# Optimization experiments

Hardware: AMD Instinct MI355X
Metric: run time of the kernel (lower is better)

## Reference

```python
import jax, jax.numpy as jnp
import numpy as np

D = 512          # descriptor_dim
H = 8            # num_heads
HD = D // H      # per-head dim
L = 12           # GNN layers: ['self','cross']*6
NAMES = ['self', 'cross'] * 6
SINKHORN_ITERS = 100
IN_EPS = 1e-5    # InstanceNorm1d eps


def _conv1x1(W, b, x):
    # W: [o, d], b: [o], x: [b, d, n] -> [b, o, n]  (1x1 Conv1d)
    return jnp.einsum('od,bdn->bon', W, x) + b[:, None]


def _instance_norm(x):
    # InstanceNorm1d(affine=False): normalize each (batch, channel) over n
    mean = jnp.mean(x, axis=-1, keepdims=True)
    var = jnp.mean(jnp.square(x - mean), axis=-1, keepdims=True)  # biased
    return (x - mean) * jax.lax.rsqrt(var + IN_EPS)


def _mha(x, src, Wq, bq, Wk, bk, Wv, bv, Wm, bm):
    # x, src: [b, D, n] / [b, D, m]; fused head-major QKV projections
    b, _, n = x.shape
    m = src.shape[2]
    q = _conv1x1(Wq, bq, x).reshape(b, H, HD, n)
    k = _conv1x1(Wk, bk, src).reshape(b, H, HD, m)
    v = _conv1x1(Wv, bv, src).reshape(b, H, HD, m)
    scores = jnp.einsum('bhdn,bhdm->bhnm', q, k) / np.float32(np.sqrt(HD))
    prob = jax.nn.softmax(scores, axis=-1)
    out = jnp.einsum('bhnm,bhdm->bhdn', prob, v)      # [b, h, hd, n]
    # torch stacks heads at dim=2 -> [b, hd, h, n], then views (b, hd*h, n):
    out = out.transpose(0, 2, 1, 3).reshape(b, D, n)  # dim-major merge order
    return _conv1x1(Wm, bm, out)


def _prop_layer(x, src, Wq, bq, Wk, bk, Wv, bv, Wm, bm, W1, b1, W2, b2):
    # AttentionalPropagation: attn message + MLP([2D, 2D, D]) with InstanceNorm
    msg = _mha(x, src, Wq, bq, Wk, bk, Wv, bv, Wm, bm)
    y = jnp.concatenate([x, msg], axis=1)             # [b, 2D, n]
    z = jax.nn.relu(_instance_norm(_conv1x1(W1, b1, y)))
    return _conv1x1(W2, b2, z)                        # [b, D, n]


def _log_optimal_transport(scores, alpha, iters):
    b, m, n = scores.shape
    ms = jnp.asarray(m, scores.dtype)
    ns = jnp.asarray(n, scores.dtype)
    bins0 = jnp.broadcast_to(alpha, (b, m, 1))
    bins1 = jnp.broadcast_to(alpha, (b, 1, n))
    a = jnp.broadcast_to(alpha, (b, 1, 1))
    couplings = jnp.concatenate(
        [jnp.concatenate([scores, bins0], -1),
         jnp.concatenate([bins1, a], -1)], 1)         # [b, m+1, n+1]
    norm = -jnp.log(ms + ns)
    log_mu = jnp.concatenate([jnp.full((m,), norm), (jnp.log(ns) + norm)[None]])
    log_nu = jnp.concatenate([jnp.full((n,), norm), (jnp.log(ms) + norm)[None]])
    log_mu = jnp.broadcast_to(log_mu, (b, m + 1))
    log_nu = jnp.broadcast_to(log_nu, (b, n + 1))

    def step(carry, _):
        u, v = carry
        u = log_mu - jax.scipy.special.logsumexp(couplings + v[:, None, :], axis=2)
        v = log_nu - jax.scipy.special.logsumexp(couplings + u[:, :, None], axis=1)
        return (u, v), None

    (u, v), _ = jax.lax.scan(
        step, (jnp.zeros_like(log_mu), jnp.zeros_like(log_nu)), None,
        length=iters)
    return couplings + u[:, :, None] + v[:, None, :] - norm


def setup_inputs() -> dict:
    key = jax.random.key(0)
    ks = jax.random.split(key, 12)
    B, N0, N1 = 4, 1024, 1024
    s = np.float32(0.03)  # ~1/sqrt(D) init scale for stability over 12 layers

    def p(k, shape):
        return jax.random.normal(k, shape, jnp.float32) * s

    return {
        'descs_0': jax.random.normal(ks[0], (B, N0, D), jnp.float32),
        'descs_1': jax.random.normal(ks[1], (B, N1, D), jnp.float32),
        'Wq': p(ks[2], (L, D, D)), 'bq': jnp.zeros((L, D), jnp.float32),
        'Wk': p(ks[3], (L, D, D)), 'bk': jnp.zeros((L, D), jnp.float32),
        'Wv': p(ks[4], (L, D, D)), 'bv': jnp.zeros((L, D), jnp.float32),
        'Wm': p(ks[5], (L, D, D)), 'bm': jnp.zeros((L, D), jnp.float32),
        'W1': p(ks[6], (L, 2 * D, 2 * D)), 'b1': jnp.zeros((L, 2 * D), jnp.float32),
        'W2': p(ks[7], (L, D, 2 * D)), 'b2': jnp.zeros((L, D), jnp.float32),
        'Wf': p(ks[8], (D, D)), 'bf': jnp.zeros((D,), jnp.float32),
        'bin_score': jnp.asarray(1.0, jnp.float32),
    }


def reference(descs_0, descs_1, Wq, bq, Wk, bk, Wv, bv, Wm, bm,
              W1, b1, W2, b2, Wf, bf, bin_score):
    # [B, N, D] -> channels-first [B, D, N]
    x0 = jnp.transpose(descs_0, (0, 2, 1))
    x1 = jnp.transpose(descs_1, (0, 2, 1))
    for i, name in enumerate(NAMES):
        s0, s1 = (x1, x0) if name == 'cross' else (x0, x1)
        args = (Wq[i], bq[i], Wk[i], bk[i], Wv[i], bv[i], Wm[i], bm[i],
                W1[i], b1[i], W2[i], b2[i])
        d0 = _prop_layer(x0, s0, *args)
        d1 = _prop_layer(x1, s1, *args)
        x0 = x0 + d0
        x1 = x1 + d1
    m0 = _conv1x1(Wf, bf, x0)
    m1 = _conv1x1(Wf, bf, x1)
    scores = jnp.einsum('bdn,bdm->bnm', m0, m1) / np.float32(np.sqrt(D))
    return _log_optimal_transport(scores, bin_score, SINKHORN_ITERS)
```

## Files before the change

kernel.cpp:

```cpp
#include <hip/hip_runtime.h>
#include <hip/hip_bf16.h>
#include <hip/hip_fp16.h>
#include <cmath>

using bf16 = __hip_bfloat16;
typedef __attribute__((ext_vector_type(8))) short short8;
typedef __attribute__((ext_vector_type(4))) short shortx4;
typedef __attribute__((ext_vector_type(4))) float floatx4;
typedef unsigned long long u64t;

__device__ __forceinline__ void lds_load16(void* lds, const void* g) {
  __builtin_amdgcn_global_load_lds(
      (const __attribute__((address_space(1))) void*)g,
      (__attribute__((address_space(3))) void*)lds, 16, 0, 0);
}

struct GemmP {
  const bf16* A; const bf16* B;
  int M, N, K, lda, ldb;
  long sAimg, sAh, sBimg, sBh;
  int ZH, cross;
  float scale;
  const float* bias;
  float* Cf; int ldcf; long sCfImg, sCfH;
  bf16* Cb; int ldcb; long sCbImg, sCbH;
  __half* Ch; int ldch; long sChImg, sChH;
  const float* resid;
  bf16* Cv; int vColOfs;
  float* statsOut;
};

template <int NTILE>
__global__ __launch_bounds__(256, 2)
void gemm_bt(GemmP p) {
  __shared__ __align__(16) bf16 As[128 * 32];
  __shared__ __align__(16) bf16 Bs[NTILE * 32];
  constexpr int MI = (NTILE == 128) ? 4 : 2;
  const int z = blockIdx.z;
  const int imgA = z / p.ZH;
  const int h = z - imgA * p.ZH;
  const int imgB = imgA ^ p.cross;
  const bf16* Ab = p.A + (long)imgA * p.sAimg + (long)h * p.sAh;
  const bf16* Bb = p.B + (long)imgB * p.sBimg + (long)h * p.sBh;
  const int m0 = blockIdx.y * 128, n0 = blockIdx.x * NTILE;
  const int t = threadIdx.x, w = t >> 6, l = t & 63;
  const int lr = l >> 2, lk = (l & 3) * 8;
  const int fr = l & 15, fk = (l >> 4) * 8;

  const bf16* aG0 = Ab + (long)(m0 + w * 16 + lr) * p.lda + lk;
  const bf16* aG1 = aG0 + (long)64 * p.lda;
  const bf16* bG0 = Bb + (long)(n0 + w * 16 + lr) * p.ldb + lk;
  const bf16* bG1 = bG0 + (long)64 * p.ldb;
  bf16* aL0 = &As[w * 16 * 32];
  bf16* aL1 = &As[(w + 4) * 16 * 32];
  bf16* bL0 = &Bs[w * 16 * 32];
  bf16* bL1 = &Bs[(w + 4) * 16 * 32];
  const int wr = (NTILE == 128) ? (w >> 1) * 64 : w * 32;
  const int wc = (NTILE == 128) ? (w & 1) * 64 : 0;

  floatx4 zero4 = {0.f, 0.f, 0.f, 0.f};
  floatx4 acc[MI][4];
#pragma unroll
  for (int i = 0; i < MI; i++)
#pragma unroll
    for (int j = 0; j < 4; j++) acc[i][j] = zero4;

  for (int k0 = 0; k0 < p.K; k0 += 32) {
    lds_load16(aL0, aG0 + k0);
    lds_load16(aL1, aG1 + k0);
    lds_load16(bL0, bG0 + k0);
    if (NTILE == 128) lds_load16(bL1, bG1 + k0);
    __syncthreads();
    short8 af[MI], bfv[4];
#pragma unroll
    for (int i = 0; i < MI; i++)
      af[i] = *(const short8*)&As[(wr + i * 16 + fr) * 32 + fk];
#pragma unroll
    for (int j = 0; j < 4; j++)
      bfv[j] = *(const short8*)&Bs[(wc + j * 16 + fr) * 32 + fk];
#pragma unroll
    for (int i = 0; i < MI; i++)
#pragma unroll
      for (int j = 0; j < 4; j++)
        acc[i][j] = __builtin_amdgcn_mfma_f32_16x16x32_bf16(af[i], bfv[j], acc[i][j], 0, 0, 0);
    __syncthreads();
  }

  const int cl = l & 15, rq = (l >> 4) * 4;
  const long cfBase = (long)imgA * p.sCfImg + (long)h * p.sCfH;
  const long cbBase = (long)imgA * p.sCbImg + (long)h * p.sCbH;
  const long chBase = (long)imgA * p.sChImg + (long)h * p.sChH;
#pragma unroll
  for (int j = 0; j < 4; j++) {
    const int col = n0 + wc + j * 16 + cl;
    if (col >= p.N) continue;
    const float bv = p.bias ? p.bias[col] : 0.f;
    const bool vcol = p.Cv && (col >= p.vColOfs);
    float cs = 0.f, cs2 = 0.f;
#pragma unroll
    for (int i = 0; i < MI; i++) {
      float vr[4];
#pragma unroll
      for (int r = 0; r < 4; r++) {
        const int row = m0 + wr + i * 16 + rq + r;
        float val = acc[i][j][r] * p.scale + bv;
        if (p.resid) val += p.resid[cfBase + (long)row * p.ldcf + col];
        if (p.Cf) p.Cf[cfBase + (long)row * p.ldcf + col] = val;
        if (p.Cb && !vcol) p.Cb[cbBase + (long)row * p.ldcb + col] = __float2bfloat16(val);
        if (p.Ch) p.Ch[chBase + (long)row * p.ldch + col] = __float2half(val);
        if (p.statsOut) { cs += val; cs2 += val * val; }
        vr[r] = val;
      }
      if (vcol) {
        const int row0 = m0 + wr + i * 16 + rq;
        const int img = row0 >> 10, tok = row0 & 1023;
        const int ch = col - p.vColOfs;
        shortx4 pk;
#pragma unroll
        for (int r = 0; r < 4; r++) {
          bf16 bb = __float2bfloat16(vr[r]);
          pk[r] = *reinterpret_cast<short*>(&bb);
        }
        *(shortx4*)(p.Cv + (long)img * 524288 + (long)ch * 1024 + tok) = pk;
      }
    }
    if (p.statsOut) {
      cs += __shfl_xor(cs, 16); cs += __shfl_xor(cs, 32);
      cs2 += __shfl_xor(cs2, 16); cs2 += __shfl_xor(cs2, 32);
      if (l < 16) {
        const int img = m0 >> 10;
        atomicAdd(&p.statsOut[img * 2048 + col], cs);
        atomicAdd(&p.statsOut[img * 2048 + 1024 + col], cs2);
      }
    }
  }
}

__global__ __launch_bounds__(256, 4)
void attn_fused(const bf16* __restrict__ QKV, const bf16* __restrict__ vchan,
                bf16* __restrict__ Yb, int cross) {
  __shared__ __align__(16) bf16 Qs[64 * 64];
  __shared__ __align__(16) bf16 Ks[64 * 64];
  __shared__ __align__(16) bf16 Vs[64 * 64];
  __shared__ __align__(16) bf16 Ps[64 * 64];
  const int z = blockIdx.z;
  const int img = z >> 3, h = z & 7;
  const int imgB = img ^ cross;
  const int q0 = blockIdx.x * 64;
  const int t = threadIdx.x, w = t >> 6, l = t & 63;
  const int g = l >> 4, fr = l & 15;
  const int wr = w * 16;

  {
    const bf16* src = QKV + ((long)(img * 1024 + q0)) * 1536 + h * 64;
#pragma unroll
    for (int k = 0; k < 2; k++) {
      const int chunk = t + k * 256;
      const int row = chunk >> 3, c16 = chunk & 7;
      const short8 vd = *(const short8*)(src + (long)row * 1536 + c16 * 8);
      *(short8*)((char*)Qs + row * 128 + ((c16 * 16) ^ ((row & 7) << 4))) = vd;
    }
  }
  __syncthreads();

  short8 qf[2];
#pragma unroll
  for (int ks = 0; ks < 2; ks++) {
    const int row = wr + fr;
    qf[ks] = *(const short8*)((const char*)Qs + row * 128 +
                              ((ks * 64 + g * 16) ^ ((row & 7) << 4)));
  }

  floatx4 zero4 = {0.f, 0.f, 0.f, 0.f};
  floatx4 Oa[4];
  float m_run[4], l_run[4];
#pragma unroll
  for (int r = 0; r < 4; r++) { m_run[r] = -3.0e38f; l_run[r] = 0.f; }
#pragma unroll
  for (int jd = 0; jd < 4; jd++) Oa[jd] = zero4;

  const bf16* ksrc0 = QKV + ((long)(imgB * 1024)) * 1536 + 512 + h * 64;
  const bf16* vsrc0 = vchan + (long)imgB * 524288 + (long)(h * 64) * 1024;

  for (int kv = 0; kv < 16; kv++) {
    const int kv0 = kv * 64;
#pragma unroll
    for (int k = 0; k < 2; k++) {
      const int ch = t + k * 256;
      const int row = ch >> 3, c16 = ch & 7;
      const short8 vd = *(const short8*)(ksrc0 + (long)(kv0 + row) * 1536 + c16 * 8);
      *(short8*)((char*)Ks + row * 128 + ((c16 * 16) ^ ((row & 7) << 4))) = vd;
    }
#pragma unroll
    for (int k = 0; k < 2; k++) {
      const int ch = t + k * 256;
      const int row = ch >> 3, c16 = ch & 7;
      const short8 vd = *(const short8*)(vsrc0 + (long)row * 1024 + kv0 + c16 * 8);
      *(short8*)((char*)Vs + row * 128 + ((c16 * 16) ^ ((row & 7) << 4))) = vd;
    }
    __syncthreads();

    floatx4 sa[4];
#pragma unroll
    for (int j = 0; j < 4; j++) {
      sa[j] = zero4;
      const int row = j * 16 + fr;
      const short8 bk0 = *(const short8*)((const char*)Ks + row * 128 +
                                          ((g * 16) ^ ((row & 7) << 4)));
      const short8 bk1 = *(const short8*)((const char*)Ks + row * 128 +
                                          ((64 + g * 16) ^ ((row & 7) << 4)));
      sa[j] = __builtin_amdgcn_mfma_f32_16x16x32_bf16(qf[0], bk0, sa[j], 0, 0, 0);
      sa[j] = __builtin_amdgcn_mfma_f32_16x16x32_bf16(qf[1], bk1, sa[j], 0, 0, 0);
    }

#pragma unroll
    for (int r = 0; r < 4; r++) {
      float mx = -3.0e38f;
#pragma unroll
      for (int j = 0; j < 4; j++) {
        sa[j][r] *= 0.125f;
        mx = fmaxf(mx, sa[j][r]);
      }
#pragma unroll
      for (int o = 1; o < 16; o <<= 1) mx = fmaxf(mx, __shfl_xor(mx, o));
      const float mnew = fmaxf(m_run[r], mx);
      const float corr = __expf(m_run[r] - mnew);
      m_run[r] = mnew;
      float ps = 0.f;
#pragma unroll
      for (int j = 0; j < 4; j++) {
        const float pv = __expf(sa[j][r] - mnew);
        sa[j][r] = pv;
        ps += pv;
      }
#pragma unroll
      for (int o = 1; o < 16; o <<= 1) ps += __shfl_xor(ps, o);
      l_run[r] = l_run[r] * corr + ps;
#pragma unroll
      for (int jd = 0; jd < 4; jd++) Oa[jd][r] *= corr;
    }

#pragma unroll
    for (int j = 0; j < 4; j++)
#pragma unroll
      for (int r = 0; r < 4; r++) {
        const int row = wr + g * 4 + r;
        const int colB = j * 32 + fr * 2;
        *(bf16*)((char*)Ps + row * 128 + (colB ^ ((row & 7) << 4))) =
            __float2bfloat16(sa[j][r]);
      }

    short8 pf[2];
#pragma unroll
    for (int ks = 0; ks < 2; ks++) {
      const int row = wr + fr;
      pf[ks] = *(const short8*)((const char*)Ps + row * 128 +
                                ((ks * 64 + g * 16) ^ ((row & 7) << 4)));
    }
#pragma unroll
    for (int jd = 0; jd < 4; jd++) {
      const int row = jd * 16 + fr;
      const short8 vf0 = *(const short8*)((const char*)Vs + row * 128 +
                                          ((g * 16) ^ ((row & 7) << 4)));
      const short8 vf1 = *(const short8*)((const char*)Vs + row * 128 +
                                          ((64 + g * 16) ^ ((row & 7) << 4)));
      Oa[jd] = __builtin_amdgcn_mfma_f32_16x16x32_bf16(pf[0], vf0, Oa[jd], 0, 0, 0);
      Oa[jd] = __builtin_amdgcn_mfma_f32_16x16x32_bf16(pf[1], vf1, Oa[jd], 0, 0, 0);
    }
    __syncthreads();
  }

#pragma unroll
  for (int r = 0; r < 4; r++) {
    const float inv = 1.f / l_run[r];
    const int qrow = q0 + wr + g * 4 + r;
    bf16* dst = Yb + ((long)img * 1024 + qrow) * 1024 + 512 + h * 64;
#pragma unroll
    for (int jd = 0; jd < 4; jd++)
      dst[jd * 16 + fr] = __float2bfloat16(Oa[jd][r] * inv);
  }
}

__global__ __launch_bounds__(256)
void cvt_f2b(const float* __restrict__ in, bf16* __restrict__ out, long n) {
  long i = (long)blockIdx.x * 256 + threadIdx.x;
  const long stride = (long)gridDim.x * 256;
  for (; i < n; i += stride) out[i] = __float2bfloat16(in[i]);
}

__global__ __launch_bounds__(256)
void cvt_prep(const float* __restrict__ W1, const float* __restrict__ Wm,
              bf16* __restrict__ w1r, bf16* __restrict__ wmT) {
  const long i = (long)blockIdx.x * 256 + threadIdx.x;
  if (i < 6291456L) {
    const int lay = (int)(i >> 19);
    const long r = i & 524287;
    const int o = (int)(r >> 9), k = (int)(r & 511);
    w1r[i] = __float2bfloat16(W1[(long)lay * 1048576 + (long)o * 1024 + 512 + k]);
  } else if (i < 9437184L) {
    const long j = i - 6291456L;
    const int lay = (int)(j >> 18);
    const long r = j & 262143;
    const int c = (int)(r >> 9), ii = (int)(r & 511);
    wmT[j] = __float2bfloat16(Wm[(long)lay * 262144 + (long)ii * 512 + (c & 63) * 8 + (c >> 6)]);
  }
}

__global__ __launch_bounds__(256)
void bc_calc(const float* __restrict__ W1, const float* __restrict__ bm,
             const float* __restrict__ b1, float* __restrict__ bc) {
  const int w = threadIdx.x >> 6, l = threadIdx.x & 63;
  const int og = blockIdx.x * 4 + w;
  const int lay = og >> 10, o = og & 1023;
  const float* wrow = W1 + (long)lay * 1048576 + (long)o * 1024 + 512;
  const float* bmr = bm + lay * 512;
  float s = 0.f;
#pragma unroll
  for (int j = 0; j < 8; j++) s += wrow[l + 64 * j] * bmr[l + 64 * j];
#pragma unroll
  for (int o2 = 32; o2 >= 1; o2 >>= 1) s += __shfl_xor(s, o2);
  if (l == 0) bc[og] = b1[og] + s;
}

__global__ __launch_bounds__(256)
void cvt_layer(const float* __restrict__ Wq, const float* __restrict__ Wk,
               const float* __restrict__ Wv, const float* __restrict__ W1,
               const float* __restrict__ W2, const bf16* __restrict__ wcAll,
               const float* __restrict__ bq, const float* __restrict__ bk,
               const float* __restrict__ bv,
               int layer, bf16* __restrict__ out, float* __restrict__ bqkv) {
  const long i = (long)blockIdx.x * 256 + threadIdx.x;
  if (i >= 2359296L + 1536) return;
  if (i >= 2359296L) {
    const int j = (int)(i - 2359296L);
    float b;
    if (j < 512) b = bq[layer * 512 + j];
    else if (j < 1024) b = bk[layer * 512 + j - 512];
    else b = bv[layer * 512 + j - 1024];
    bqkv[j] = b;
    return;
  }
  if (i < 786432) {
    float v;
    if (i < 262144) v = Wq[(long)layer * 262144 + i];
    else if (i < 524288) v = Wk[(long)layer * 262144 + i - 262144];
    else v = Wv[(long)layer * 262144 + i - 524288];
    out[i] = __float2bfloat16(v);
  } else if (i < 1835008) {
    const long j = i - 786432;
    const int o = (int)(j >> 10), k = (int)(j & 1023);
    if (k < 512)
      out[i] = __float2bfloat16(W1[(long)layer * 1048576 + (long)o * 1024 + k]);
    else
      out[i] = wcAll[(long)layer * 524288 + (long)o * 512 + (k - 512)];
  } else {
    const long j = i - 1835008;
    out[i] = __float2bfloat16(W2[(long)layer * 524288 + j]);
  }
}

__global__ __launch_bounds__(256)
void init_x(const float* __restrict__ d0, const float* __restrict__ d1,
            float* __restrict__ Xf, bf16* __restrict__ Yb) {
  long i = (long)blockIdx.x * 256 + threadIdx.x;
  const long stride = (long)gridDim.x * 256;
  const long n = 8L * 1024 * 512;
  for (; i < n; i += stride) {
    const int d = (int)(i & 511);
    const long nn = i >> 9;
    const int img = (int)(nn >> 10);
    const int row = (int)(nn & 1023);
    const int b = img >> 1, s = img & 1;
    const float v = (s ? d1 : d0)[((long)b * 1024 + row) * 512 + d];
    Xf[i] = v;
    Yb[(nn << 10) + d] = __float2bfloat16(v);
  }
}

__global__ __launch_bounds__(256)
void in_apply(const float* __restrict__ T1, const float* __restrict__ stats,
              bf16* __restrict__ Z) {
  long i = (long)blockIdx.x * 256 + threadIdx.x;
  const long stride = (long)gridDim.x * 256;
  for (; i < 8L * 1024 * 1024; i += stride) {
    const int c = (int)(i & 1023);
    const int img = (int)(i >> 20);
    const float mean = stats[img * 2048 + c] * (1.f / 1024.f);
    const float var = fmaxf(stats[img * 2048 + 1024 + c] * (1.f / 1024.f) - mean * mean, 0.f);
    const float zz = (T1[i] - mean) * rsqrtf(var + 1e-5f);
    Z[i] = __float2bfloat16(fmaxf(zz, 0.f));
  }
}

__global__ __launch_bounds__(256)
void coup_to_fp16(float* __restrict__ io, const float* __restrict__ alpha,
                  __half* __restrict__ outN, __half* __restrict__ outT) {
  __shared__ float tile[32][33];
  const float a = *alpha;
  const int b = blockIdx.z;
  const int x0 = blockIdx.x * 32, y0 = blockIdx.y * 32;
  const int lx = threadIdx.x & 31, ly = threadIdx.x >> 5;
#pragma unroll
  for (int i = 0; i < 4; i++) {
    const int y = ly + i * 8;
    if (y0 + y < 1025 && x0 + lx < 1025) {
      const long idx = ((long)b * 1025 + y0 + y) * 1025 + x0 + lx;
      const bool edge = (y0 + y == 1024) || (x0 + lx == 1024);
      float vv;
      if (edge) { vv = a; io[idx] = a; }
      else vv = io[idx];
      tile[y][lx] = vv;
      outN[idx] = __float2half(vv);
    }
  }
  __syncthreads();
#pragma unroll
  for (int i = 0; i < 4; i++) {
    const int y = ly + i * 8;
    if (x0 + y < 1025 && y0 + lx < 1025)
      outT[((long)b * 1025 + x0 + y) * 1025 + y0 + lx] = __float2half(tile[lx][y]);
  }
}

#define SK_BLOCKS 256

#define SK_ROUND(CREG, CLAST, XREG, XLAST, SRC, DST)                            \
  {                                                                             \
    u64t pr;                                                                    \
    while ((unsigned)((pr = __hip_atomic_load(&(SRC)[t], __ATOMIC_RELAXED,      \
                                              __HIP_MEMORY_SCOPE_AGENT)) >>    \
                      32) != tag)                                               \
      __builtin_amdgcn_s_sleep(1);                                              \
    sv[t] = __uint_as_float((unsigned)pr);                                      \
    if (t == 0) {                                                               \
      u64t qr;                                                                  \
      while ((unsigned)((qr = __hip_atomic_load(&(SRC)[1024], __ATOMIC_RELAXED, \
                                                __HIP_MEMORY_SCOPE_AGENT)) >>  \
                        32) != tag)                                             \
        __builtin_amdgcn_s_sleep(1);                                            \
      sv[1024] = __uint_as_float((unsigned)qr);                                 \
    }                                                                           \
    __syncthreads();                                                            \
    float M = (l == 0) ? ((CLAST) + sv[1024]) : -3.0e38f;                       \
    const float extra = M;                                                      \
    float x[16];                                                                \
    _Pragma("unroll") for (int i = 0; i < 16; i++) {                            \
      x[i] = (CREG)[i] + sv[l + 64 * i];                                        \
      M = fmaxf(M, x[i]);                                                       \
    }                                                                           \
    _Pragma("unroll") for (int o = 32; o >= 1; o >>= 1)                         \
        M = fmaxf(M, __shfl_xor(M, o));                                         \
    float S = (l == 0) ? __expf(extra - M) : 0.f;                               \
    _Pragma("unroll") for (int i = 0; i < 16; i++) S += __expf(x[i] - M);       \
    _Pragma("unroll") for (int o = 32; o >= 1; o >>= 1) S += __shfl_xor(S, o);  \
    if (l == 0) {                                                               \
      const float val = norm - (M + __logf(S));                                 \
      const u64t pk = ((u64t)(tag + 1) << 32) | (u64t)__float_as_uint(val);     \
      __hip_atomic_store(&(DST)[lw], pk, __ATOMIC_RELAXED,                      \
                         __HIP_MEMORY_SCOPE_AGENT);                             \
    }                                                                           \
    if (xtra) {                                                                 \
      float M2 = (l == 0) ? ((XLAST) + sv[1024]) : -3.0e38f;                    \
      const float e2 = M2;                                                      \
      float y[16];                                                              \
      _Pragma("unroll") for (int i = 0; i < 16; i++) {                          \
        y[i] = (XREG)[i] + sv[l + 64 * i];                                      \
        M2 = fmaxf(M2, y[i]);                                                   \
      }                                                                         \
      _Pragma("unroll") for (int o = 32; o >= 1; o >>= 1)                       \
          M2 = fmaxf(M2, __shfl_xor(M2, o));                                    \
      float S2 = (l == 0) ? __expf(e2 - M2) : 0.f;                              \
      _Pragma("unroll") for (int i = 0; i < 16; i++) S2 += __expf(y[i] - M2);   \
      _Pragma("unroll") for (int o = 32; o >= 1; o >>= 1)                       \
          S2 += __shfl_xor(S2, o);                                              \
      if (l == 0) {                                                             \
        const float v2 = (logN + norm) - (M2 + __logf(S2));                     \
        const u64t pk2 = ((u64t)(tag + 1) << 32) | (u64t)__float_as_uint(v2);   \
        __hip_atomic_store(&(DST)[1024], pk2, __ATOMIC_RELAXED,                 \
                           __HIP_MEMORY_SCOPE_AGENT);                           \
      }                                                                         \
    }                                                                           \
    tag++;                                                                      \
    __syncthreads();                                                            \
  }

__global__ __launch_bounds__(1024)
void sinkhorn_pers(const __half* __restrict__ C, const __half* __restrict__ CT,
                   u64t* __restrict__ u, u64t* __restrict__ v,
                   float norm, float logN, int iters) {
  __shared__ float sv[1025];
  const int t = threadIdx.x;
  const int w = t >> 6, l = t & 63;
  const int b = blockIdx.x >> 6;
  const int kb = blockIdx.x & 63;
  const int lw = kb * 16 + w;
  const __half* Cb = C + (long)b * 1050625;
  const __half* CTb = CT + (long)b * 1050625;
  u64t* ub = u + b * 1025;
  u64t* vb = v + b * 1025;

  float cr[16], cc[16];
  float clC, clT;
  {
    const __half* rc = Cb + (long)lw * 1025;
    const __half* rt = CTb + (long)lw * 1025;
#pragma unroll
    for (int i = 0; i < 16; i++) {
      cr[i] = __half2float(rc[l + 64 * i]);
      cc[i] = __half2float(rt[l + 64 * i]);
    }
    clC = (l == 0) ? __half2float(rc[1024]) : 0.f;
    clT = (l == 0) ? __half2float(rt[1024]) : 0.f;
  }
  const bool xtra = (lw == 0);
  float xrC[16], xrT[16], xlC = 0.f, xlT = 0.f;
  if (xtra) {
    const __half* rc = Cb + (long)1024 * 1025;
    const __half* rt = CTb + (long)1024 * 1025;
#pragma unroll
    for (int i = 0; i < 16; i++) {
      xrC[i] = __half2float(rc[l + 64 * i]);
      xrT[i] = __half2float(rt[l + 64 * i]);
    }
    if (l == 0) {
      xlC = __half2float(rc[1024]);
      xlT = __half2float(rt[1024]);
    }
  }

  unsigned tag = 0;
  for (int it = 0; it < iters; it++) {
    SK_ROUND(cr, clC, xrC, xlC, vb, ub);
    SK_ROUND(cc, clT, xrT, xlT, ub, vb);
  }
}

__global__ __launch_bounds__(256)
void ot_final(float* __restrict__ C, const u64t* __restrict__ u,
              const u64t* __restrict__ v, float norm) {
  long i = (long)blockIdx.x * 256 + threadIdx.x;
  if (i >= 4L * 1025 * 1025) return;
  const int b = (int)(i / 1050625);
  const long r = i - (long)b * 1050625;
  const int n = (int)(r / 1025);
  const int m = (int)(r - (long)n * 1025);
  const float uu = __uint_as_float((unsigned)u[b * 1025 + n]);
  const float vv = __uint_as_float((unsigned)v[b * 1025 + m]);
  C[i] += uu + vv - norm;
}

extern "C" void kernel_launch(void* const* d_in, const int* in_sizes, int n_in,
                              void* d_out, int out_size, void* d_ws, size_t ws_size,
                              hipStream_t stream) {
  (void)in_sizes; (void)n_in; (void)out_size; (void)ws_size;
  const float* descs0 = (const float*)d_in[0];
  const float* descs1 = (const float*)d_in[1];
  const float* Wq = (const float*)d_in[2];
  const float* bq = (const float*)d_in[3];
  const float* Wk = (const float*)d_in[4];
  const float* bk = (const float*)d_in[5];
  const float* Wv = (const float*)d_in[6];
  const float* bvv = (const float*)d_in[7];
  const float* Wm = (const float*)d_in[8];
  const float* bm = (const float*)d_in[9];
  const float* W1 = (const float*)d_in[10];
  const float* b1 = (const float*)d_in[11];
  const float* W2 = (const float*)d_in[12];
  const float* b2 = (const float*)d_in[13];
  const float* Wf = (const float*)d_in[14];
  const float* bff = (const float*)d_in[15];
  const float* alpha = (const float*)d_in[16];

  char* ws = (char*)d_ws;
  size_t off = 0;
  auto alloc = [&](size_t bytes) -> void* {
    off = (off + 255) & ~(size_t)255;
    void* p = ws + off;
    off += bytes;
    return p;
  };

  bf16* wL = (bf16*)alloc(2359296L * 2);
  float* bqkv = (float*)alloc(1536 * 4);
  bf16* WfB = (bf16*)alloc(512L * 512 * 2);
  bf16* wcAll = (bf16*)alloc(12L * 1024 * 512 * 2);
  float* bcAll = (float*)alloc(12L * 1024 * 4);
  float* Xf = (float*)alloc(8L * 1024 * 512 * 4);
  bf16* Yb = (bf16*)alloc(8L * 1024 * 1024 * 2);
  bf16* QKVb = (bf16*)alloc(8L * 1024 * 1536 * 2);
  bf16* vchan = (bf16*)alloc(8L * 1024 * 512 * 2);
  char* SCR = (char*)alloc(50331648);
  float* stats = (float*)alloc(12L * 16384 * 4);
  u64t* u = (u64t*)alloc(4L * 1025 * 8);
  u64t* v = (u64t*)alloc(4L * 1025 * 8);

  bf16* wqkv = wL;
  bf16* w1m = wL + 786432;
  bf16* w2 = wL + 1835008;
  float* T1 = (float*)SCR;
  bf16* Zb = (bf16*)(SCR + 33554432);
  bf16* w1rTmp = (bf16*)SCR;
  bf16* wmTTmp = (bf16*)(SCR + 12582912);
  __half* Ch = (__half*)SCR;
  __half* CTh = (__half*)(SCR + 8405248);
  bf16* mproj = (bf16*)(SCR + 33554432);
  float* coup = (float*)d_out;

  cvt_f2b<<<512, 256, 0, stream>>>(Wf, WfB, 512L * 512);
  init_x<<<4096, 256, 0, stream>>>(descs0, descs1, Xf, Yb);
  hipMemsetAsync(stats, 0, 12L * 16384 * 4, stream);

  auto gemm = [&](int ntile, const bf16* A, const bf16* B, int M, int N, int K,
                  int lda, int ldb, long sAimg, long sAh, long sBimg, long sBh,
                  int Z, int ZH, int cross, float scale, const float* bias,
                  float* Cf, int ldcf, long sCfImg, long sCfH,
                  bf16* Cb, int ldcb, long sCbImg, long sCbH,
                  __half* Ch_, int ldch, long sChImg, long sChH,
                  const float* resid, bf16* Cv, int vColOfs, float* statsOut) {
    GemmP p;
    p.A = A; p.B = B; p.M = M; p.N = N; p.K = K; p.lda = lda; p.ldb = ldb;
    p.sAimg = sAimg; p.sAh = sAh; p.sBimg = sBimg; p.sBh = sBh;
    p.ZH = ZH; p.cross = cross; p.scale = scale; p.bias = bias;
    p.Cf = Cf; p.ldcf = ldcf; p.sCfImg = sCfImg; p.sCfH = sCfH;
    p.Cb = Cb; p.ldcb = ldcb; p.sCbImg = sCbImg; p.sCbH = sCbH;
    p.Ch = Ch_; p.ldch = ldch; p.sChImg = sChImg; p.sChH = sChH;
    p.resid = resid; p.Cv = Cv; p.vColOfs = vColOfs; p.statsOut = statsOut;
    dim3 g((unsigned)((N + ntile - 1) / ntile), (unsigned)((M + 127) / 128), (unsigned)Z);
    if (ntile == 128) gemm_bt<128><<<g, 256, 0, stream>>>(p);
    else gemm_bt<64><<<g, 256, 0, stream>>>(p);
  };

  cvt_prep<<<36864, 256, 0, stream>>>(W1, Wm, w1rTmp, wmTTmp);
  bc_calc<<<3072, 256, 0, stream>>>(W1, bm, b1, bcAll);
  gemm(128, w1rTmp, wmTTmp, 1024, 512, 512, 512, 512, 524288, 0, 262144, 0,
       12, 1, 0, 1.f, nullptr,
       nullptr, 0, 0, 0, wcAll, 512, 524288, 0, nullptr, 0, 0, 0,
       nullptr, nullptr, 0, nullptr);

  for (int i = 0; i < 12; i++) {
    const int cross = i & 1;
    cvt_layer<<<9222, 256, 0, stream>>>(Wq, Wk, Wv, W1, W2, wcAll, bq, bk, bvv, i, wL, bqkv);

    gemm(128, Yb, wqkv, 8192, 1536, 512, 1024, 512, 0, 0, 0, 0, 1, 1, 0, 1.f, bqkv,
         nullptr, 0, 0, 0, QKVb, 1536, 0, 0, nullptr, 0, 0, 0,
         nullptr, vchan, 1024, nullptr);
    attn_fused<<<dim3(16, 1, 64), 256, 0, stream>>>(QKVb, vchan, Yb, cross);

    gemm(128, Yb, w1m, 8192, 1024, 1024, 1024, 1024, 0, 0, 0, 0, 1, 1, 0, 1.f,
         bcAll + i * 1024,
         T1, 1024, 0, 0, nullptr, 0, 0, 0, nullptr, 0, 0, 0,
         nullptr, nullptr, 0, stats + (long)i * 16384);
    in_apply<<<8192, 256, 0, stream>>>(T1, stats + (long)i * 16384, Zb);
    gemm(128, Zb, w2, 8192, 512, 1024, 1024, 1024, 0, 0, 0, 0, 1, 1, 0, 1.f, b2 + i * 512,
         Xf, 512, 0, 0, Yb, 1024, 0, 0, nullptr, 0, 0, 0,
         Xf, nullptr, 0, nullptr);
  }

  gemm(128, Yb, WfB, 8192, 512, 512, 1024, 512, 0, 0, 0, 0, 1, 1, 0, 1.f, bff,
       nullptr, 0, 0, 0, mproj, 512, 0, 0, nullptr, 0, 0, 0,
       nullptr, nullptr, 0, nullptr);
  gemm(128, mproj, mproj + 524288, 1024, 1024, 512, 512, 512,
       1048576, 0, 1048576, 0, 4, 1, 0,
       0.044194173824159216f, nullptr,
       coup, 1025, 1050625, 0, nullptr, 0, 0, 0, nullptr, 0, 0, 0,
       nullptr, nullptr, 0, nullptr);
  coup_to_fp16<<<dim3(33, 33, 4), 256, 0, stream>>>(coup, alpha, Ch, CTh);

  hipMemsetAsync(u, 0, 4L * 1025 * 8, stream);
  hipMemsetAsync(v, 0, 4L * 1025 * 8, stream);
  const float NORM = -logf(2048.f);
  const float LOGN = logf(1024.f);
  int iters = 100;
  void* args[] = {(void*)&Ch, (void*)&CTh, (void*)&u, (void*)&v,
                  (void*)&NORM, (void*)&LOGN, (void*)&iters};
  hipLaunchCooperativeKernel((void*)sinkhorn_pers, dim3(SK_BLOCKS), dim3(1024), args, 0, stream);
  ot_final<<<16417, 256, 0, stream>>>(coup, u, v, NORM);
}
```

Baseline: 3.182 ms.

## Remap GEMM workgroups across XCDs, vectorize instance-norm apply, narrow N tiles

Adds a block-ID remap for 2D GEMM grids that spreads consecutive workgroups across the 8 XCDs in strided chunks, meant to improve L2 locality. The instance-norm apply kernel now handles four elements per thread with float4 loads and 4-wide bf16 stores, cutting instruction count and memory transactions. The W2 and final projection GEMMs (N=512) switch to 64-wide N tiles, giving more workgroups to fill the CUs at the cost of less reuse per tile.

New measurement: 2.933 ms. 7.8% less time.

```diff
diff --git a/kernel.cpp b/kernel.cpp
--- a/kernel.cpp
+++ b/kernel.cpp
@@ -42,7 +42,18 @@
   const int imgB = imgA ^ p.cross;
   const bf16* Ab = p.A + (long)imgA * p.sAimg + (long)h * p.sAh;
   const bf16* Bb = p.B + (long)imgB * p.sBimg + (long)h * p.sBh;
-  const int m0 = blockIdx.y * 128, n0 = blockIdx.x * NTILE;
+
+  int bx = blockIdx.x, by = blockIdx.y;
+  if (gridDim.z == 1) {
+    const unsigned nwg = gridDim.x * gridDim.y;
+    if ((nwg & 7u) == 0) {
+      const unsigned id = blockIdx.y * gridDim.x + blockIdx.x;
+      const unsigned nid = (id & 7u) * (nwg >> 3) + (id >> 3);
+      bx = nid % gridDim.x;
+      by = nid / gridDim.x;
+    }
+  }
+  const int m0 = by * 128, n0 = bx * NTILE;
   const int t = threadIdx.x, w = t >> 6, l = t & 63;
   const int lr = l >> 2, lk = (l & 3) * 8;
   const int fr = l & 15, fk = (l >> 4) * 8;
@@ -382,13 +393,23 @@
               bf16* __restrict__ Z) {
   long i = (long)blockIdx.x * 256 + threadIdx.x;
   const long stride = (long)gridDim.x * 256;
-  for (; i < 8L * 1024 * 1024; i += stride) {
-    const int c = (int)(i & 1023);
-    const int img = (int)(i >> 20);
-    const float mean = stats[img * 2048 + c] * (1.f / 1024.f);
-    const float var = fmaxf(stats[img * 2048 + 1024 + c] * (1.f / 1024.f) - mean * mean, 0.f);
-    const float zz = (T1[i] - mean) * rsqrtf(var + 1e-5f);
-    Z[i] = __float2bfloat16(fmaxf(zz, 0.f));
+  for (; i < 2L * 1024 * 1024; i += stride) {
+    const float4 tv = *(const float4*)(T1 + i * 4);
+    const int c0 = (int)((i * 4) & 1023);
+    const int img = (int)(i >> 18);
+    const float* st = stats + img * 2048;
+    float vv[4] = {tv.x, tv.y, tv.z, tv.w};
+    shortx4 zo;
+#pragma unroll
+    for (int k = 0; k < 4; k++) {
+      const int c = c0 + k;
+      const float mean = st[c] * (1.f / 1024.f);
+      const float var = fmaxf(st[1024 + c] * (1.f / 1024.f) - mean * mean, 0.f);
+      const float zz = (vv[k] - mean) * rsqrtf(var + 1e-5f);
+      bf16 bb = __float2bfloat16(fmaxf(zz, 0.f));
+      zo[k] = *reinterpret_cast<short*>(&bb);
+    }
+    *(shortx4*)(Z + i * 4) = zo;
   }
 }
 
@@ -650,13 +671,13 @@
          bcAll + i * 1024,
          T1, 1024, 0, 0, nullptr, 0, 0, 0, nullptr, 0, 0, 0,
          nullptr, nullptr, 0, stats + (long)i * 16384);
-    in_apply<<<8192, 256, 0, stream>>>(T1, stats + (long)i * 16384, Zb);
-    gemm(128, Zb, w2, 8192, 512, 1024, 1024, 1024, 0, 0, 0, 0, 1, 1, 0, 1.f, b2 + i * 512,
+    in_apply<<<2048, 256, 0, stream>>>(T1, stats + (long)i * 16384, Zb);
+    gemm(64, Zb, w2, 8192, 512, 1024, 1024, 1024, 0, 0, 0, 0, 1, 1, 0, 1.f, b2 + i * 512,
          Xf, 512, 0, 0, Yb, 1024, 0, 0, nullptr, 0, 0, 0,
          Xf, nullptr, 0, nullptr);
   }
 
-  gemm(128, Yb, WfB, 8192, 512, 512, 1024, 512, 0, 0, 0, 0, 1, 1, 0, 1.f, bff,
+  gemm(64, Yb, WfB, 8192, 512, 512, 1024, 512, 0, 0, 0, 0, 1, 1, 0, 1.f, bff,
        nullptr, 0, 0, 0, mproj, 512, 0, 0, nullptr, 0, 0, 0,
        nullptr, nullptr, 0, nullptr);
   gemm(128, mproj, mproj + 524288, 1024, 1024, 512, 512, 512,
```
